# Optimization experiments

Hardware: AMD Instinct MI355X
Metric: run time of the kernel (lower is better)

## Reference

```python
import jax, jax.numpy as jnp
import numpy as np

G = 8          # num_groups
GIN = 2048 // G   # group_in_features
GOUT = 2048 // G  # group_out_features


def setup_inputs() -> dict:
    key = jax.random.key(0)
    kx, kw, kb = jax.random.split(key, 3)
    x = jax.random.normal(kx, (8192, 2048), dtype=jnp.float32)
    # per-group linear params, torch nn.Linear default init scale ~ U(-1/sqrt(fan_in), ...)
    bound = 1.0 / np.sqrt(GIN)
    W = jax.random.uniform(kw, (G, GIN, GOUT), minval=-bound, maxval=bound, dtype=jnp.float32)
    b = jax.random.uniform(kb, (G, GOUT), minval=-bound, maxval=bound, dtype=jnp.float32)
    # rational activation coeffs, init p=[1,0,0,0], q=[1,0,0] per group
    p = jnp.tile(jnp.array([1.0, 0.0, 0.0, 0.0], dtype=jnp.float32), (G, 1))
    q = jnp.tile(jnp.array([1.0, 0.0, 0.0], dtype=jnp.float32), (G, 1))
    return {"x": x, "W": W, "b": b, "p": p, "q": q}


def _rational(y, p, q):
    # y: [N, G, GOUT]; p: [G, 4]; q: [G, 3] -> broadcast over N and GOUT
    p = p[None, :, :, None]  # [1,G,4,1]
    q = q[None, :, :, None]  # [1,G,3,1]
    y2 = y * y
    y3 = y2 * y
    num = p[:, :, 0] + p[:, :, 1] * y + p[:, :, 2] * y2 + p[:, :, 3] * y3
    den = 1.0 + jnp.abs(q[:, :, 0] * y + q[:, :, 1] * y2 + q[:, :, 2] * y3)
    return num / den


def reference(x, W, b, p, q):
    N = x.shape[0]
    xg = x.reshape(N, G, GIN)                       # chunk along last dim
    y = jnp.einsum('ngi,gio->ngo', xg, W) + b[None]  # grouped GEMM, [N,G,GOUT]
    out = _rational(y, p, q)
    return out.reshape(N, G * GOUT)                 # cat along last dim
```

## Files before the change

kernel.cpp:

```cpp
#include <hip/hip_runtime.h>
#include <hip/hip_bf16.h>

#define G_ 8
#define GIN_ 256
#define GOUT_ 256
#define NROWS_ 8192
#define LDX_ 2048

typedef __attribute__((ext_vector_type(4))) float f32x4;
typedef __attribute__((ext_vector_type(8))) short bf16x8;

__global__ __launch_bounds__(256) void wprep_kernel(const float* __restrict__ W,
                                                    __hip_bfloat16* __restrict__ Wt) {
    __shared__ float tile[64][65];
    const int bid = blockIdx.x;
    const int g  = bid >> 4;
    const int ot = (bid >> 2) & 3;
    const int it = bid & 3;
    const float* Wg = W + g * GIN_ * GOUT_;
    __hip_bfloat16* Wtg = Wt + g * GIN_ * GOUT_;
    const int lane_o = threadIdx.x & 63;
    const int sub    = threadIdx.x >> 6;
#pragma unroll
    for (int r = 0; r < 16; ++r) {
        int i = r * 4 + sub;
        tile[i][lane_o] = Wg[(it * 64 + i) * GOUT_ + ot * 64 + lane_o];
    }
    __syncthreads();
#pragma unroll
    for (int r = 0; r < 16; ++r) {
        int o = r * 4 + sub;
        Wtg[(ot * 64 + o) * GIN_ + it * 64 + lane_o] = __float2bfloat16(tile[lane_o][o]);
    }
}

__global__ __launch_bounds__(256) void gkan_kernel(const float* __restrict__ x,
                                                   const __hip_bfloat16* __restrict__ Wt,
                                                   const float* __restrict__ bias,
                                                   const float* __restrict__ pc,
                                                   const float* __restrict__ qc,
                                                   float* __restrict__ out) {
    __shared__ __align__(16) __hip_bfloat16 As[128 * 32];
    __shared__ __align__(16) __hip_bfloat16 Bs[128 * 32];

    const int bid   = blockIdx.x;
    const int mtile = bid & 63;
    const int nid   = bid >> 6;
    const int g     = nid >> 1;
    const int ntile = nid & 1;

    const int m0 = mtile * 128;
    const int n0 = ntile * 128;

    const int t    = threadIdx.x;
    const int wave = t >> 6;
    const int lane = t & 63;
    const int lm   = lane & 15;
    const int quad = lane >> 4;
    const int wrow = wave >> 1;
    const int wcol = wave & 1;

    const float* xg = x + (size_t)m0 * LDX_ + g * GIN_;
    const __hip_bfloat16* Wtg = Wt + (size_t)g * GIN_ * GOUT_ + (size_t)n0 * GIN_;

    f32x4 acc[4][4] = {};

    const int qd0 = wave * 2;
    const int bn_sub = lane >> 2;
    const int bk_sub = lane & 3;

    for (int kk = 0; kk < 8; ++kk) {
        const int k0 = kk * 32;

#pragma unroll
        for (int s = 0; s < 2; ++s) {
            const int qd = qd0 + s;
            const int nloc = qd * 16 + bn_sub;
            const __hip_bfloat16* src = Wtg + nloc * GIN_ + k0 + bk_sub * 8;
            __builtin_amdgcn_global_load_lds(
                (const __attribute__((address_space(1))) unsigned int*)src,
                (__attribute__((address_space(3))) unsigned int*)(Bs + qd * 512),
                16, 0, 0);
        }

#pragma unroll
        for (int itc = 0; itc < 4; ++itc) {
            const int c    = itc * 256 + t;
            const int row  = c >> 3;
            const int col4 = c & 7;
            const f32x4 v = *(const f32x4*)(xg + (size_t)row * LDX_ + k0 + col4 * 4);
            union { __hip_bfloat16 h[4]; unsigned long long u; } cv;
            cv.h[0] = __float2bfloat16(v.x);
            cv.h[1] = __float2bfloat16(v.y);
            cv.h[2] = __float2bfloat16(v.z);
            cv.h[3] = __float2bfloat16(v.w);
            *(unsigned long long*)(As + row * 32 + col4 * 4) = cv.u;
        }

        __syncthreads();

        bf16x8 af[4], bf[4];
#pragma unroll
        for (int mt = 0; mt < 4; ++mt)
            af[mt] = *(const bf16x8*)(As + (wrow * 64 + mt * 16 + lm) * 32 + quad * 8);
#pragma unroll
        for (int nt = 0; nt < 4; ++nt)
            bf[nt] = *(const bf16x8*)(Bs + (wcol * 64 + nt * 16 + lm) * 32 + quad * 8);
#pragma unroll
        for (int mt = 0; mt < 4; ++mt)
#pragma unroll
            for (int nt = 0; nt < 4; ++nt)
                acc[mt][nt] = __builtin_amdgcn_mfma_f32_16x16x32_bf16(
                    af[mt], bf[nt], acc[mt][nt], 0, 0, 0);

        __syncthreads();
    }

    const float p0 = pc[g * 4 + 0], p1 = pc[g * 4 + 1];
    const float p2 = pc[g * 4 + 2], p3 = pc[g * 4 + 3];
    const float q0 = qc[g * 3 + 0], q1 = qc[g * 3 + 1], q2 = qc[g * 3 + 2];

#pragma unroll
    for (int nt = 0; nt < 4; ++nt) {
        const int col = n0 + wcol * 64 + nt * 16 + lm;
        const float bb = bias[g * GOUT_ + col];
#pragma unroll
        for (int mt = 0; mt < 4; ++mt) {
#pragma unroll
            for (int r = 0; r < 4; ++r) {
                const int row = m0 + wrow * 64 + mt * 16 + quad * 4 + r;
                const float y  = acc[mt][nt][r] + bb;
                const float num = p0 + y * (p1 + y * (p2 + y * p3));
                const float den = 1.0f + fabsf(y * (q0 + y * (q1 + y * q2)));
                out[(size_t)row * LDX_ + g * GOUT_ + col] = num * __builtin_amdgcn_rcpf(den);
            }
        }
    }
}

extern "C" void kernel_launch(void* const* d_in, const int* in_sizes, int n_in,
                              void* d_out, int out_size, void* d_ws, size_t ws_size,
                              hipStream_t stream) {
    const float* x = (const float*)d_in[0];
    const float* W = (const float*)d_in[1];
    const float* b = (const float*)d_in[2];
    const float* p = (const float*)d_in[3];
    const float* q = (const float*)d_in[4];
    float* out = (float*)d_out;

    __hip_bfloat16* Wt = (__hip_bfloat16*)d_ws;

    wprep_kernel<<<128, 256, 0, stream>>>(W, Wt);
    gkan_kernel<<<1024, 256, 0, stream>>>(x, Wt, b, p, q, out);
}
```

Before: 144.7 us.

## Hold full weight tile in registers and stream x directly without LDS

The GEMM kernel drops shared memory and barriers. Each wave preloads its whole 64-column by 256-k bf16 weight slice into registers and loads x fragments straight from global memory into MFMA operand layout, with register double buffering. Tiles shrink to 128x64 per block and 32 rows per wave, doubling the grid. The cost is heavy register pressure (128 VGPRs for weights), lower reuse of x across output columns so x is read more times from memory, and uncoalesced-ish per-lane row loads.

```diff
diff --git a/kernel.cpp b/kernel.cpp
--- a/kernel.cpp
+++ b/kernel.cpp
@@ -34,86 +34,80 @@
     }
 }
 
-__global__ __launch_bounds__(256) void gkan_kernel(const float* __restrict__ x,
-                                                   const __hip_bfloat16* __restrict__ Wt,
-                                                   const float* __restrict__ bias,
-                                                   const float* __restrict__ pc,
-                                                   const float* __restrict__ qc,
-                                                   float* __restrict__ out) {
-    __shared__ __align__(16) __hip_bfloat16 As[128 * 32];
-    __shared__ __align__(16) __hip_bfloat16 Bs[128 * 32];
-
+__global__ __launch_bounds__(256, 2) void gkan_kernel(const float* __restrict__ x,
+                                                      const __hip_bfloat16* __restrict__ Wt,
+                                                      const float* __restrict__ bias,
+                                                      const float* __restrict__ pc,
+                                                      const float* __restrict__ qc,
+                                                      float* __restrict__ out) {
     const int bid   = blockIdx.x;
-    const int mtile = bid & 63;
-    const int nid   = bid >> 6;
-    const int g     = nid >> 1;
-    const int ntile = nid & 1;
-
-    const int m0 = mtile * 128;
-    const int n0 = ntile * 128;
+    const int mtile = bid >> 5;
+    const int ntile = bid & 31;
+    const int g     = ntile >> 2;
+    const int n0    = (ntile & 3) * 64;
 
     const int t    = threadIdx.x;
     const int wave = t >> 6;
     const int lane = t & 63;
     const int lm   = lane & 15;
     const int quad = lane >> 4;
-    const int wrow = wave >> 1;
-    const int wcol = wave & 1;
 
-    const float* xg = x + (size_t)m0 * LDX_ + g * GIN_;
-    const __hip_bfloat16* Wtg = Wt + (size_t)g * GIN_ * GOUT_ + (size_t)n0 * GIN_;
+    const int m0 = mtile * 128 + wave * 32;
 
-    f32x4 acc[4][4] = {};
+    bf16x8 Bfr[8][4];
+    {
+        const __hip_bfloat16* Wg = Wt + (size_t)g * (GIN_ * GOUT_);
+#pragma unroll
+        for (int nt = 0; nt < 4; ++nt) {
+            const __hip_bfloat16* Wn = Wg + (size_t)(n0 + nt * 16 + lm) * GIN_ + quad * 8;
+#pragma unroll
+            for (int kk = 0; kk < 8; ++kk)
+                Bfr[kk][nt] = *(const bf16x8*)(Wn + kk * 32);
+        }
+    }
 
-    const int qd0 = wave * 2;
-    const int bn_sub = lane >> 2;
-    const int bk_sub = lane & 3;
+    const float* xr0 = x + (size_t)(m0 + lm) * LDX_ + g * GIN_ + quad * 8;
+    const float* xr1 = xr0 + (size_t)16 * LDX_;
 
-    for (int kk = 0; kk < 8; ++kk) {
-        const int k0 = kk * 32;
+    f32x4 acc[2][4] = {};
+
+    f32x4 ra[2][2][2];
+    ra[0][0][0] = *(const f32x4*)(xr0);
+    ra[0][0][1] = *(const f32x4*)(xr0 + 4);
+    ra[0][1][0] = *(const f32x4*)(xr1);
+    ra[0][1][1] = *(const f32x4*)(xr1 + 4);
 
 #pragma unroll
-        for (int s = 0; s < 2; ++s) {
-            const int qd = qd0 + s;
-            const int nloc = qd * 16 + bn_sub;
-            const __hip_bfloat16* src = Wtg + nloc * GIN_ + k0 + bk_sub * 8;
-            __builtin_amdgcn_global_load_lds(
-                (const __attribute__((address_space(1))) unsigned int*)src,
-                (__attribute__((address_space(3))) unsigned int*)(Bs + qd * 512),
-                16, 0, 0);
+    for (int kk = 0; kk < 8; ++kk) {
+        const int cur = kk & 1, nxt = cur ^ 1;
+        if (kk < 7) {
+            const int ko = (kk + 1) * 32;
+            ra[nxt][0][0] = *(const f32x4*)(xr0 + ko);
+            ra[nxt][0][1] = *(const f32x4*)(xr0 + ko + 4);
+            ra[nxt][1][0] = *(const f32x4*)(xr1 + ko);
+            ra[nxt][1][1] = *(const f32x4*)(xr1 + ko + 4);
         }
-
+        bf16x8 af[2];
 #pragma unroll
-        for (int itc = 0; itc < 4; ++itc) {
-            const int c    = itc * 256 + t;
-            const int row  = c >> 3;
-            const int col4 = c & 7;
-            const f32x4 v = *(const f32x4*)(xg + (size_t)row * LDX_ + k0 + col4 * 4);
-            union { __hip_bfloat16 h[4]; unsigned long long u; } cv;
-            cv.h[0] = __float2bfloat16(v.x);
-            cv.h[1] = __float2bfloat16(v.y);
-            cv.h[2] = __float2bfloat16(v.z);
-            cv.h[3] = __float2bfloat16(v.w);
-            *(unsigned long long*)(As + row * 32 + col4 * 4) = cv.u;
+        for (int mt = 0; mt < 2; ++mt) {
+            const f32x4 a0 = ra[cur][mt][0], a1 = ra[cur][mt][1];
+            union { __hip_bfloat16 h[8]; bf16x8 v; } cv;
+            cv.h[0] = __float2bfloat16(a0.x);
+            cv.h[1] = __float2bfloat16(a0.y);
+            cv.h[2] = __float2bfloat16(a0.z);
+            cv.h[3] = __float2bfloat16(a0.w);
+            cv.h[4] = __float2bfloat16(a1.x);
+            cv.h[5] = __float2bfloat16(a1.y);
+            cv.h[6] = __float2bfloat16(a1.z);
+            cv.h[7] = __float2bfloat16(a1.w);
+            af[mt] = cv.v;
         }
-
-        __syncthreads();
-
-        bf16x8 af[4], bf[4];
 #pragma unroll
-        for (int mt = 0; mt < 4; ++mt)
-            af[mt] = *(const bf16x8*)(As + (wrow * 64 + mt * 16 + lm) * 32 + quad * 8);
-#pragma unroll
-        for (int nt = 0; nt < 4; ++nt)
-            bf[nt] = *(const bf16x8*)(Bs + (wcol * 64 + nt * 16 + lm) * 32 + quad * 8);
-#pragma unroll
-        for (int mt = 0; mt < 4; ++mt)
+        for (int mt = 0; mt < 2; ++mt)
 #pragma unroll
             for (int nt = 0; nt < 4; ++nt)
                 acc[mt][nt] = __builtin_amdgcn_mfma_f32_16x16x32_bf16(
-                    af[mt], bf[nt], acc[mt][nt], 0, 0, 0);
-
-        __syncthreads();
+                    af[mt], Bfr[kk][nt], acc[mt][nt], 0, 0, 0);
     }
 
     const float p0 = pc[g * 4 + 0], p1 = pc[g * 4 + 1];
@@ -122,14 +116,14 @@
 
 #pragma unroll
     for (int nt = 0; nt < 4; ++nt) {
-        const int col = n0 + wcol * 64 + nt * 16 + lm;
+        const int col = n0 + nt * 16 + lm;
         const float bb = bias[g * GOUT_ + col];
 #pragma unroll
-        for (int mt = 0; mt < 4; ++mt) {
+        for (int mt = 0; mt < 2; ++mt) {
 #pragma unroll
             for (int r = 0; r < 4; ++r) {
-                const int row = m0 + wrow * 64 + mt * 16 + quad * 4 + r;
-                const float y  = acc[mt][nt][r] + bb;
+                const int row = m0 + mt * 16 + quad * 4 + r;
+                const float y   = acc[mt][nt][r] + bb;
                 const float num = p0 + y * (p1 + y * (p2 + y * p3));
                 const float den = 1.0f + fabsf(y * (q0 + y * (q1 + y * q2)));
                 out[(size_t)row * LDX_ + g * GOUT_ + col] = num * __builtin_amdgcn_rcpf(den);
@@ -151,5 +145,5 @@
     __hip_bfloat16* Wt = (__hip_bfloat16*)d_ws;
 
     wprep_kernel<<<128, 256, 0, stream>>>(W, Wt);
-    gkan_kernel<<<1024, 256, 0, stream>>>(x, Wt, b, p, q, out);
+    gkan_kernel<<<2048, 256, 0, stream>>>(x, Wt, b, p, q, out);
 }
```

Measured after the change: 172.3 us. +19.1%, slower.
